# Kernel optimization log

Hardware: AMD Instinct MI355X
Metric: run time of the kernel (lower is better)

## Reference

```python
import jax, jax.numpy as jnp
import numpy as np

H = 64  # hidden size
I = 1   # input size


def setup_inputs() -> dict:
    key = jax.random.key(0)
    ks = jax.random.split(key, 7)
    B, T = 4096, 512
    s_ih = 1.0 / np.sqrt(H)
    x = jax.random.normal(ks[0], (B, T, I), dtype=jnp.float32)
    # torch nn.GRU params: weight_ih [3H, I], weight_hh [3H, H], biases [3H]
    W_ih = jax.random.uniform(ks[1], (3 * H, I), minval=-s_ih, maxval=s_ih, dtype=jnp.float32)
    W_hh = jax.random.uniform(ks[2], (3 * H, H), minval=-s_ih, maxval=s_ih, dtype=jnp.float32)
    b_ih = jax.random.uniform(ks[3], (3 * H,), minval=-s_ih, maxval=s_ih, dtype=jnp.float32)
    b_hh = jax.random.uniform(ks[4], (3 * H,), minval=-s_ih, maxval=s_ih, dtype=jnp.float32)
    # final Linear(64, 1)
    W_out = jax.random.uniform(ks[5], (1, H), minval=-s_ih, maxval=s_ih, dtype=jnp.float32)
    b_out = jax.random.uniform(ks[6], (1,), minval=-s_ih, maxval=s_ih, dtype=jnp.float32)
    return {"x": x, "W_ih": W_ih, "W_hh": W_hh, "b_ih": b_ih, "b_hh": b_hh,
            "W_out": W_out, "b_out": b_out}


def _gru_last_hidden(x, W_ih, W_hh, b_ih, b_hh):
    B, T, _ = x.shape
    # precompute input projections for all timesteps: [B, T, 3H]
    xp = jnp.einsum('bti,gi->btg', x, W_ih) + b_ih
    xp = jnp.swapaxes(xp, 0, 1)  # [T, B, 3H]
    Whr, Whz, Whn = W_hh[:H], W_hh[H:2 * H], W_hh[2 * H:]
    bhr, bhz, bhn = b_hh[:H], b_hh[H:2 * H], b_hh[2 * H:]

    def step(h, xt):
        xr, xz, xn = xt[:, :H], xt[:, H:2 * H], xt[:, 2 * H:]
        r = jax.nn.sigmoid(xr + h @ Whr.T + bhr)
        z = jax.nn.sigmoid(xz + h @ Whz.T + bhz)
        n = jnp.tanh(xn + r * (h @ Whn.T + bhn))
        h_new = (1.0 - z) * n + z * h
        return h_new, None

    h0 = jnp.zeros((B, H), dtype=x.dtype)
    h_last, _ = jax.lax.scan(step, h0, xp)
    return h_last


def reference(x, W_ih, W_hh, b_ih, b_hh, W_out, b_out):
    h_last = _gru_last_hidden(x, W_ih, W_hh, b_ih, b_hh)
    return h_last @ W_out.T + b_out  # [B, 1]
```

## Files before the change

kernel.cpp:

```cpp
#include <hip/hip_runtime.h>
#include <stdint.h>

#define TT 512
#define BT 8

typedef float    f32x4 __attribute__((ext_vector_type(4)));
typedef float    f32x2 __attribute__((ext_vector_type(2)));
typedef short    s16x8 __attribute__((ext_vector_type(8)));
typedef _Float16 f16x8 __attribute__((ext_vector_type(8)));

#define MFMA_F16(A, B, C) \
    __builtin_amdgcn_mfma_f32_16x16x32_f16( \
        __builtin_bit_cast(f16x8, (A)), (B), (C), 0, 0, 0)

#define LOG2E  1.442695040888963f
#define LOG2E2 2.885390081777927f

__global__ __launch_bounds__(256, 2) void gru_scan_kernel(
    const float* __restrict__ x,
    const float* __restrict__ Wih,
    const float* __restrict__ Whh,
    const float* __restrict__ bih,
    const float* __restrict__ bhh,
    const float* __restrict__ Wout,
    const float* __restrict__ bout,
    float* __restrict__ out)
{
    __shared__ __align__(16) float xs2[TT * BT];
    __shared__ __align__(16) short hbuf[2][1024];
    __shared__ float outp[4][BT];

    const int tid  = threadIdx.x;
    const int w    = tid >> 6;
    const int L    = tid & 63;
    const int n16  = L & 15;
    const int quad = L >> 4;
    const int q    = w * 16 + n16;
    const int b0   = blockIdx.x * BT;

    #pragma unroll
    for (int k = 0; k < 4; ++k) {
        int idx = tid + k * 256;
        int row = idx >> 7;
        int t4  = idx & 127;
        f32x4 v = *(const f32x4*)(x + (size_t)(b0 + row) * TT + t4 * 4);
        #pragma unroll
        for (int i = 0; i < 4; ++i)
            xs2[(t4 * 4 + i) * BT + row] = v[i];
    }
    {
        f32x4* hb = (f32x4*)hbuf;
        f32x4 zv = {0.f, 0.f, 0.f, 0.f};
        hb[tid] = zv;
    }

    const float wr2   = -LOG2E  * Wih[q];
    const float wz2   = -LOG2E  * Wih[64 + q];
    const float wn2   =  LOG2E2 * Wih[128 + q];
    const float bR2   = -LOG2E  * (bih[q]      + bhh[q]);
    const float bZ2   = -LOG2E  * (bih[64 + q] + bhh[64 + q]);
    const float bN2   =  LOG2E2 * bhh[128 + q];
    const float bihn2 =  LOG2E2 * bih[128 + q];
    const float wo    = Wout[q];

    const f32x4 bR4 = {bR2, bR2, bR2, bR2};
    const f32x4 bZ4 = {bZ2, bZ2, bZ2, bZ2};
    const f32x4 bN4 = {bN2, bN2, bN2, bN2};

    f16x8 Bf[3][2];
    #pragma unroll
    for (int g = 0; g < 3; ++g) {
        const float sg = (g == 2) ? LOG2E2 : -LOG2E;
        #pragma unroll
        for (int c = 0; c < 2; ++c) {
            const float* p = Whh + ((g * 64 + q) * 64 + c * 32 + quad * 8);
            #pragma unroll
            for (int j = 0; j < 8; ++j)
                Bf[g][c][j] = (_Float16)(p[j] * sg);
        }
    }

    float hD[2] = {0.f, 0.f};

    const int kg   = q >> 3;
    const int sxor = (kg & 1) * 4;
    int waddr[2];
    #pragma unroll
    for (int p = 0; p < 2; ++p)
        waddr[p] = (kg * 16 + ((p * 4 + quad) ^ sxor)) * 8 + (q & 7);

    const int permx = ((n16 & 3) * 4 + (n16 >> 2)) ^ ((quad & 1) * 4);
    const int rslot = quad * 16 + permx;

    const s16x8* hbv = (const s16x8*)hbuf;

    auto step = [&](int cur, int t) {
        __syncthreads();

        s16x8 A0 = hbv[cur * 128 +  0 + rslot];
        s16x8 A1 = hbv[cur * 128 + 64 + rslot];
        f32x2 xv = *(const f32x2*)(xs2 + t * BT + quad * 2);

        f32x4 aR = MFMA_F16(A0, Bf[0][0], bR4);
        aR       = MFMA_F16(A1, Bf[0][1], aR);
        f32x4 aN = MFMA_F16(A0, Bf[2][0], bN4);
        aN       = MFMA_F16(A1, Bf[2][1], aN);
        f32x4 aZ = MFMA_F16(A0, Bf[1][0], bZ4);
        aZ       = MFMA_F16(A1, Bf[1][1], aZ);

        short* wh = (short*)hbuf + (cur ^ 1) * 1024;

        f32x2 aRp = {aR[0], aR[1]};
        f32x2 aZp = {aZ[0], aZ[1]};
        f32x2 aNp = {aN[0], aN[1]};
        f32x2 hp  = {hD[0], hD[1]};

        f32x2 ar = xv * wr2 + aRp;
        f32x2 Er = {__builtin_amdgcn_exp2f(ar[0]), __builtin_amdgcn_exp2f(ar[1])};
        f32x2 DR = Er + 1.0f;
        f32x2 r  = {__builtin_amdgcn_rcpf(DR[0]), __builtin_amdgcn_rcpf(DR[1])};
        f32x2 az = xv * wz2 + aZp;
        f32x2 Ez = {__builtin_amdgcn_exp2f(az[0]), __builtin_amdgcn_exp2f(az[1])};
        f32x2 DZ = Ez + 1.0f;
        f32x2 xn = xv * wn2 + bihn2;
        f32x2 an = r * aNp + xn;
        f32x2 En = {__builtin_amdgcn_exp2f(an[0]), __builtin_amdgcn_exp2f(an[1])};
        f32x2 DN = En + 1.0f;
        f32x2 P  = DZ * DN;
        f32x2 iq = {__builtin_amdgcn_rcpf(P[0]), __builtin_amdgcn_rcpf(P[1])};
        f32x2 z  = iq * DN;
        f32x2 rn = iq * DZ;
        f32x2 n  = rn * -2.0f + 1.0f;
        f32x2 hn = z * (hp - n) + n;

        hD[0] = hn[0]; hD[1] = hn[1];

        wh[waddr[0]] = __builtin_bit_cast(short, (_Float16)hn[0]);
        wh[waddr[1]] = __builtin_bit_cast(short, (_Float16)hn[1]);
    };

    for (int t = 0; t < TT; t += 2) {
        step(0, t);
        step(1, t + 1);
    }

    float p0 = hD[0] * wo;
    float p1 = hD[1] * wo;
    #pragma unroll
    for (int mask = 1; mask <= 8; mask <<= 1) {
        p0 += __shfl_xor(p0, mask, 64);
        p1 += __shfl_xor(p1, mask, 64);
    }
    if (n16 == 0) {
        outp[w][quad * 2]     = p0;
        outp[w][quad * 2 + 1] = p1;
    }
    __syncthreads();
    if (tid < BT) {
        out[b0 + tid] = outp[0][tid] + outp[1][tid] + outp[2][tid] + outp[3][tid] + bout[0];
    }
}

extern "C" void kernel_launch(void* const* d_in, const int* in_sizes, int n_in,
                              void* d_out, int out_size, void* d_ws, size_t ws_size,
                              hipStream_t stream) {
    (void)in_sizes; (void)n_in; (void)d_ws; (void)ws_size; (void)out_size;
    const float* x    = (const float*)d_in[0];
    const float* Wih  = (const float*)d_in[1];
    const float* Whh  = (const float*)d_in[2];
    const float* bih  = (const float*)d_in[3];
    const float* bhh  = (const float*)d_in[4];
    const float* Wout = (const float*)d_in[5];
    const float* bout = (const float*)d_in[6];
    float* out = (float*)d_out;

    gru_scan_kernel<<<dim3(4096 / BT), dim3(256), 0, stream>>>(
        x, Wih, Whh, bih, bhh, Wout, bout, out);
}
```

Baseline: 200.8 us.

## Fold input projection into MFMA accumulator init, vectorize x loads, stagger blocks

Stores x row-major in LDS with a padded stride, so each lane loads four timesteps at once and the loop unrolls by four. The r and z input projections are now computed before the barrier and passed in as the MFMA accumulator initial values, which takes work off the critical path after the matmul. The fp16 conversion of h uses a single packed round-toward-zero convert instead of two separate ones. Half of the blocks also start with a short s_sleep to stagger them. Round-toward-zero changes numerics slightly, and the sleep is a speculative scheduling tweak.

Result: slower. 210.3 us (+4.7%).

```diff
diff --git a/kernel.cpp b/kernel.cpp
--- a/kernel.cpp
+++ b/kernel.cpp
@@ -3,10 +3,12 @@
 
 #define TT 512
 #define BT 8
+#define XSTR 516
 
 typedef float    f32x4 __attribute__((ext_vector_type(4)));
 typedef float    f32x2 __attribute__((ext_vector_type(2)));
 typedef short    s16x8 __attribute__((ext_vector_type(8)));
+typedef __fp16   h16x2 __attribute__((ext_vector_type(2)));
 typedef _Float16 f16x8 __attribute__((ext_vector_type(8)));
 
 #define MFMA_F16(A, B, C) \
@@ -26,7 +28,7 @@
     const float* __restrict__ bout,
     float* __restrict__ out)
 {
-    __shared__ __align__(16) float xs2[TT * BT];
+    __shared__ __align__(16) float xs[BT * XSTR];
     __shared__ __align__(16) short hbuf[2][1024];
     __shared__ float outp[4][BT];
 
@@ -44,9 +46,7 @@
         int row = idx >> 7;
         int t4  = idx & 127;
         f32x4 v = *(const f32x4*)(x + (size_t)(b0 + row) * TT + t4 * 4);
-        #pragma unroll
-        for (int i = 0; i < 4; ++i)
-            xs2[(t4 * 4 + i) * BT + row] = v[i];
+        *(f32x4*)(xs + row * XSTR + t4 * 4) = v;
     }
     {
         f32x4* hb = (f32x4*)hbuf;
@@ -62,10 +62,6 @@
     const float bN2   =  LOG2E2 * bhh[128 + q];
     const float bihn2 =  LOG2E2 * bih[128 + q];
     const float wo    = Wout[q];
-
-    const f32x4 bR4 = {bR2, bR2, bR2, bR2};
-    const f32x4 bZ4 = {bZ2, bZ2, bZ2, bZ2};
-    const f32x4 bN4 = {bN2, bN2, bN2, bN2};
 
     f16x8 Bf[3][2];
     #pragma unroll
@@ -93,19 +89,28 @@
     const int rslot = quad * 16 + permx;
 
     const s16x8* hbv = (const s16x8*)hbuf;
+    const float* xrow0 = xs + (quad * 2) * XSTR;
+    const float* xrow1 = xrow0 + XSTR;
 
-    auto step = [&](int cur, int t) {
+    if ((blockIdx.x >> 8) & 1) __builtin_amdgcn_s_sleep(6);
+
+    auto step = [&](int cur, f32x2 xv) {
+        f32x2 cr2 = xv * wr2 + bR2;
+        f32x2 cz2 = xv * wz2 + bZ2;
+        f32x4 cR = {cr2[0], cr2[1], cr2[0], cr2[1]};
+        f32x4 cZ = {cz2[0], cz2[1], cz2[0], cz2[1]};
+        f32x4 cN = {bN2, bN2, bN2, bN2};
+
         __syncthreads();
 
         s16x8 A0 = hbv[cur * 128 +  0 + rslot];
         s16x8 A1 = hbv[cur * 128 + 64 + rslot];
-        f32x2 xv = *(const f32x2*)(xs2 + t * BT + quad * 2);
 
-        f32x4 aR = MFMA_F16(A0, Bf[0][0], bR4);
+        f32x4 aR = MFMA_F16(A0, Bf[0][0], cR);
         aR       = MFMA_F16(A1, Bf[0][1], aR);
-        f32x4 aN = MFMA_F16(A0, Bf[2][0], bN4);
+        f32x4 aN = MFMA_F16(A0, Bf[2][0], cN);
         aN       = MFMA_F16(A1, Bf[2][1], aN);
-        f32x4 aZ = MFMA_F16(A0, Bf[1][0], bZ4);
+        f32x4 aZ = MFMA_F16(A0, Bf[1][0], cZ);
         aZ       = MFMA_F16(A1, Bf[1][1], aZ);
 
         short* wh = (short*)hbuf + (cur ^ 1) * 1024;
@@ -115,12 +120,10 @@
         f32x2 aNp = {aN[0], aN[1]};
         f32x2 hp  = {hD[0], hD[1]};
 
-        f32x2 ar = xv * wr2 + aRp;
-        f32x2 Er = {__builtin_amdgcn_exp2f(ar[0]), __builtin_amdgcn_exp2f(ar[1])};
+        f32x2 Er = {__builtin_amdgcn_exp2f(aRp[0]), __builtin_amdgcn_exp2f(aRp[1])};
         f32x2 DR = Er + 1.0f;
         f32x2 r  = {__builtin_amdgcn_rcpf(DR[0]), __builtin_amdgcn_rcpf(DR[1])};
-        f32x2 az = xv * wz2 + aZp;
-        f32x2 Ez = {__builtin_amdgcn_exp2f(az[0]), __builtin_amdgcn_exp2f(az[1])};
+        f32x2 Ez = {__builtin_amdgcn_exp2f(aZp[0]), __builtin_amdgcn_exp2f(aZp[1])};
         f32x2 DZ = Ez + 1.0f;
         f32x2 xn = xv * wn2 + bihn2;
         f32x2 an = r * aNp + xn;
@@ -135,13 +138,19 @@
 
         hD[0] = hn[0]; hD[1] = hn[1];
 
-        wh[waddr[0]] = __builtin_bit_cast(short, (_Float16)hn[0]);
-        wh[waddr[1]] = __builtin_bit_cast(short, (_Float16)hn[1]);
+        h16x2 hpk = __builtin_amdgcn_cvt_pkrtz(hn[0], hn[1]);
+        unsigned upk = __builtin_bit_cast(unsigned, hpk);
+        wh[waddr[0]] = (short)(upk & 0xffffu);
+        wh[waddr[1]] = (short)(upk >> 16);
     };
 
-    for (int t = 0; t < TT; t += 2) {
-        step(0, t);
-        step(1, t + 1);
+    for (int t = 0; t < TT; t += 4) {
+        f32x4 xa = *(const f32x4*)(xrow0 + t);
+        f32x4 xb = *(const f32x4*)(xrow1 + t);
+        step(0, f32x2{xa[0], xb[0]});
+        step(1, f32x2{xa[1], xb[1]});
+        step(0, f32x2{xa[2], xb[2]});
+        step(1, f32x2{xa[3], xb[3]});
     }
 
     float p0 = hD[0] * wo;
```
